# Kernel tuning notes

Hardware: AMD Instinct MI355X
Metric: run time of the kernel (lower is better)

Reference implementation:

```python
import jax, jax.numpy as jnp
import numpy as np

N_NODES = 100000


def sage_conv(x, edge_index, W_l, W_r, b):
    # PyG SAGEConv (aggr='mean', root_weight=True):
    # out_i = (mean_{j in N(i)} x_j) @ W_l + x_i @ W_r + b
    src, dst = edge_index[0], edge_index[1]
    msgs = x[src]                                             # [E, F] gather
    summed = jax.ops.segment_sum(msgs, dst, num_segments=N_NODES)
    deg = jax.ops.segment_sum(jnp.ones((edge_index.shape[1],), x.dtype), dst,
                              num_segments=N_NODES)
    mean = summed / jnp.maximum(deg, 1.0)[:, None]            # [N, F]
    return mean @ W_l + x @ W_r + b


def setup_inputs() -> dict:
    key = jax.random.key(0)
    ks = jax.random.split(key, 12)
    F, H = 128, 128
    E = 1600000
    s = lambda k, shp, fan: jax.random.normal(k, shp, jnp.float32) / np.sqrt(fan)
    return {
        "x": jax.random.normal(ks[0], (N_NODES, F), jnp.float32),
        "edge_index": jax.random.randint(ks[1], (2, E), 0, N_NODES, jnp.int64),
        "W1_l": s(ks[2], (F, H), F), "W1_r": s(ks[3], (F, H), F),
        "b1": jnp.zeros((H,), jnp.float32),
        "W2_l": s(ks[4], (H, H), H), "W2_r": s(ks[5], (H, H), H),
        "b2": jnp.zeros((H,), jnp.float32),
        "W3_l": s(ks[6], (H, 1), H), "W3_r": s(ks[7], (H, 1), H),
        "b3": jnp.zeros((1,), jnp.float32),
    }


def reference(x, edge_index, W1_l, W1_r, b1, W2_l, W2_r, b2, W3_l, W3_r, b3):
    h = jax.nn.relu(sage_conv(x, edge_index, W1_l, W1_r, b1))
    h = jax.nn.relu(sage_conv(h, edge_index, W2_l, W2_r, b2))
    h = sage_conv(h, edge_index, W3_l, W3_r, b3)   # [N, 1]
    return h.mean(axis=1)                          # [N]
```

## Files before the change

kernel.cpp:

```cpp
#include <hip/hip_runtime.h>


#define NN 100000
#define NB 391
#define SLAB 5120

typedef short bf16x8 __attribute__((ext_vector_type(8)));
typedef float f32x4 __attribute__((ext_vector_type(4)));

static __device__ __forceinline__ float uaf(unsigned u) { return __uint_as_float(u); }
static __device__ __forceinline__ unsigned short f2bf(float f) {
  unsigned u = __float_as_uint(f);
  u += 0x7fffu + ((u >> 16) & 1u);
  return (unsigned short)(u >> 16);
}

__global__ __launch_bounds__(256) void k_prep(
    const int* __restrict__ src, const int* __restrict__ dst, int E, int SB,
    int* __restrict__ cursor, unsigned* __restrict__ pairs,
    const float* __restrict__ x, unsigned short* __restrict__ Z1,
    unsigned short* __restrict__ Z2,
    const float* __restrict__ W1l, const float* __restrict__ W1r,
    const float* __restrict__ W2l, const float* __restrict__ W2r,
    unsigned short* __restrict__ wt1h, unsigned short* __restrict__ wt1l,
    unsigned short* __restrict__ wt2h, unsigned short* __restrict__ wt2l) {
  __shared__ int h[NB];
  __shared__ int rb[NB];
  const int b = blockIdx.x;
  const int tid = threadIdx.x;
  const int XB = NN * 16 / 256;

  if (b < SB) {
    for (int i = tid; i < NB; i += 256) h[i] = 0;
    __syncthreads();
    int s[8], d[8];
    const int base = b * 2048 + tid * 8;
    #pragma unroll
    for (int i = 0; i < 8; i++) {
      int g = base + i;
      bool ok = g < E;
      s[i] = ok ? src[g] : 0;
      d[i] = ok ? dst[g] : -1;
      if (ok) atomicAdd(&h[d[i] >> 8], 1);
    }
    __syncthreads();
    for (int i = tid; i < NB; i += 256) {
      rb[i] = h[i] ? atomicAdd(&cursor[i], h[i]) : 0;
      h[i] = 0;
    }
    __syncthreads();
    #pragma unroll
    for (int i = 0; i < 8; i++) {
      if (d[i] >= 0) {
        int bk = d[i] >> 8;
        int off = rb[bk] + atomicAdd(&h[bk], 1);
        if (off < SLAB)
          pairs[(size_t)bk * SLAB + off] =
              ((unsigned)(d[i] & 255) << 17) | (unsigned)s[i];
      }
    }
  } else if (b < SB + XB) {
    int t = (b - SB) * 256 + tid;
    int node = t >> 4, c = t & 15;
    const float4* xp = (const float4*)(x + (size_t)node * 128 + c * 8);
    float4 a = xp[0], bb = xp[1];
    float v[8] = {a.x, a.y, a.z, a.w, bb.x, bb.y, bb.z, bb.w};
    unsigned hh[8];
    #pragma unroll
    for (int i = 0; i < 8; i++) hh[i] = f2bf(v[i]);
    uint4 p;
    p.x = hh[0] | (hh[1] << 16); p.y = hh[2] | (hh[3] << 16);
    p.z = hh[4] | (hh[5] << 16); p.w = hh[6] | (hh[7] << 16);
    *(uint4*)(Z1 + (size_t)node * 256 + 128 + c * 8) = p;
  } else if (b < SB + XB + 64) {
    #pragma unroll
    for (int it = 0; it < 4; it++) {
      int t = (b - SB - XB) * 1024 + it * 256 + tid;
      int layer = t >> 15;
      int rem = t & 32767;
      int k = rem >> 7;
      int nn = rem & 127;
      const float* Wl = layer ? W2l : W1l;
      const float* Wr = layer ? W2r : W1r;
      float v = (k < 128) ? Wl[k * 128 + nn] : Wr[(k - 128) * 128 + nn];
      unsigned short hv = f2bf(v);
      unsigned short lv = f2bf(v - uaf(((unsigned)hv) << 16));
      const int frag = (nn >> 4) * 8 + (k >> 7) * 4 + ((k >> 5) & 3);
      const int lane = ((k >> 3) & 3) * 16 + (nn & 15);
      const int addr = frag * 512 + lane * 8 + (k & 7);
      (layer ? wt2h : wt1h)[addr] = hv;
      (layer ? wt2l : wt1l)[addr] = lv;
    }
  } else {
    unsigned* z1r = (unsigned*)(Z1 + (size_t)NN * 256);
    unsigned* z2r = (unsigned*)(Z2 + (size_t)NN * 256);
    if (tid < 128) z1r[tid] = 0;
    else z2r[tid - 128] = 0;
  }
}

__global__ __launch_bounds__(256) void k_build(const unsigned* __restrict__ pairs,
                                               const int* __restrict__ cursor,
                                               int* __restrict__ beg, int* __restrict__ deg,
                                               int* __restrict__ csr, int N) {
  __shared__ int cnt[256];
  __shared__ int sd[256];
  __shared__ int cur[256];
  const int b = blockIdx.x;
  const int tid = threadIdx.x;
  const size_t p0 = (size_t)b * SLAB;
  int count = cursor[b];
  if (count > SLAB) count = SLAB;
  cnt[tid] = 0;
  cur[tid] = 0;
  __syncthreads();
  for (int i = tid; i < count; i += 256) atomicAdd(&cnt[pairs[p0 + i] >> 17], 1);
  __syncthreads();
  int v = cnt[tid];
  sd[tid] = v;
  __syncthreads();
  #pragma unroll
  for (int off = 1; off < 256; off <<= 1) {
    int u = (tid >= off) ? sd[tid - off] : 0;
    __syncthreads();
    sd[tid] += u;
    __syncthreads();
  }
  const int node = b * 256 + tid;
  if (node < N) {
    beg[node] = (int)p0 + (sd[tid] - v);
    deg[node] = v;
  }
  __syncthreads();
  for (int i = tid; i < count; i += 256) {
    unsigned pv = pairs[p0 + i];
    int dl = pv >> 17;
    int pos = (sd[dl] - cnt[dl]) + atomicAdd(&cur[dl], 1);
    csr[p0 + pos] = pv & 0x1ffff;
  }
}

#define ACC8(v)                                   \
  acc[0] += uaf((v).x << 16);                     \
  acc[1] += uaf((v).x & 0xffff0000u);             \
  acc[2] += uaf((v).y << 16);                     \
  acc[3] += uaf((v).y & 0xffff0000u);             \
  acc[4] += uaf((v).z << 16);                     \
  acc[5] += uaf((v).z & 0xffff0000u);             \
  acc[6] += uaf((v).w << 16);                     \
  acc[7] += uaf((v).w & 0xffff0000u);

__global__ __launch_bounds__(256) void k_aggZ(unsigned short* __restrict__ Z,
                                              const int* __restrict__ begA,
                                              const int* __restrict__ degA,
                                              const int* __restrict__ csr, int n) {
  const int wid = (blockIdx.x * blockDim.x + threadIdx.x) >> 6;
  const int lane = threadIdx.x & 63;
  if (wid >= n) return;
  const int beg = begA[wid];
  const int d = degA[wid];
  const int g = lane >> 4, c = lane & 15;
  float acc[8] = {0.f, 0.f, 0.f, 0.f, 0.f, 0.f, 0.f, 0.f};

  for (int base = 0; base < d; base += 64) {
    int m = d - base;
    if (m > 64) m = 64;
    int idx = csr[beg + base + (lane < m ? lane : 0)];
    for (int k = 0; k < m; k += 32) {
      uint4 vA[4], vB[4];
      const bool hasB = (k + 16) < m;
      #pragma unroll
      for (int u = 0; u < 4; u++) {
        int kk = k + u * 4 + g;
        int j = __shfl(idx, kk & 63);
        j = (kk < m) ? j : NN;
        vA[u] = *(const uint4*)(Z + (size_t)j * 256 + 128 + c * 8);
      }
      if (hasB) {
        #pragma unroll
        for (int u = 0; u < 4; u++) {
          int kk = k + 16 + u * 4 + g;
          int j = __shfl(idx, kk & 63);
          j = (kk < m) ? j : NN;
          vB[u] = *(const uint4*)(Z + (size_t)j * 256 + 128 + c * 8);
        }
      }
      #pragma unroll
      for (int u = 0; u < 4; u++) { ACC8(vA[u]); }
      if (hasB) {
        #pragma unroll
        for (int u = 0; u < 4; u++) { ACC8(vB[u]); }
      }
    }
  }
  #pragma unroll
  for (int j = 0; j < 8; j++) {
    acc[j] += __shfl_xor(acc[j], 16);
    acc[j] += __shfl_xor(acc[j], 32);
  }
  const float inv = d > 0 ? 1.0f / (float)d : 0.f;
  if (g == 0) {
    unsigned h[8];
    #pragma unroll
    for (int j = 0; j < 8; j++) h[j] = f2bf(acc[j] * inv);
    uint4 p;
    p.x = h[0] | (h[1] << 16); p.y = h[2] | (h[3] << 16);
    p.z = h[4] | (h[5] << 16); p.w = h[6] | (h[7] << 16);
    *(uint4*)(Z + (size_t)wid * 256 + c * 8) = p;
  }
}

template <int MODE>
__global__ __launch_bounds__(256, 2) void k_sage2(
    const unsigned short* __restrict__ Z, const unsigned short* __restrict__ WTh,
    const unsigned short* __restrict__ WTl, const float* __restrict__ bias,
    unsigned short* __restrict__ outB,
    const float* __restrict__ w3l, const float* __restrict__ w3r,
    float* __restrict__ s2, float* __restrict__ r2, int n) {
  const int tid = threadIdx.x;
  const int lane = tid & 63;
  const int w = tid >> 6;
  const int ln = lane & 15;
  const int r16 = lane >> 4;
  const int m0 = blockIdx.x * 256 + w * 64;

  f32x4 acc[4][8];
  #pragma unroll
  for (int s = 0; s < 4; s++)
    #pragma unroll
    for (int cc = 0; cc < 8; cc++) {
      acc[s][cc][0] = 0.f; acc[s][cc][1] = 0.f;
      acc[s][cc][2] = 0.f; acc[s][cc][3] = 0.f;
    }
  float4 bv4[8];
  #pragma unroll
  for (int cc = 0; cc < 8; cc++) bv4[cc] = *(const float4*)(bias + cc * 16 + r16 * 4);

  #pragma unroll
  for (int kh = 0; kh < 2; kh++) {
    bf16x8 a[4][4];
    #pragma unroll
    for (int s = 0; s < 4; s++) {
      int row = m0 + s * 16 + ln;
      if (row > n - 1) row = n - 1;
      const unsigned short* zp = Z + (size_t)row * 256 + kh * 128 + r16 * 8;
      #pragma unroll
      for (int ks = 0; ks < 4; ks++) a[s][ks] = *(const bf16x8*)(zp + ks * 32);
    }
    #pragma unroll
    for (int ks = 0; ks < 4; ks++) {
      #pragma unroll
      for (int cg = 0; cg < 4; cg++) {
        bf16x8 bh[2], bl[2];
        #pragma unroll
        for (int j = 0; j < 2; j++) {
          const size_t o = (size_t)(((cg * 2 + j) * 8 + kh * 4 + ks) * 512 + lane * 8);
          bh[j] = *(const bf16x8*)(WTh + o);
          bl[j] = *(const bf16x8*)(WTl + o);
        }
        #pragma unroll
        for (int j = 0; j < 2; j++) {
          #pragma unroll
          for (int s = 0; s < 4; s++) {
            acc[s][cg * 2 + j] =
                __builtin_amdgcn_mfma_f32_16x16x32_bf16(bh[j], a[s][ks], acc[s][cg * 2 + j], 0, 0, 0);
            acc[s][cg * 2 + j] =
                __builtin_amdgcn_mfma_f32_16x16x32_bf16(bl[j], a[s][ks], acc[s][cg * 2 + j], 0, 0, 0);
          }
        }
      }
    }
  }

  if (MODE == 0) {
    #pragma unroll
    for (int s = 0; s < 4; s++) {
      const int node = m0 + s * 16 + ln;
      if (node < n) {
        unsigned short* op = outB + (size_t)node * 256 + 128 + r16 * 4;
        #pragma unroll
        for (int cc = 0; cc < 8; cc++) {
          ushort4 hq;
          hq.x = f2bf(fmaxf(acc[s][cc][0] + bv4[cc].x, 0.f));
          hq.y = f2bf(fmaxf(acc[s][cc][1] + bv4[cc].y, 0.f));
          hq.z = f2bf(fmaxf(acc[s][cc][2] + bv4[cc].z, 0.f));
          hq.w = f2bf(fmaxf(acc[s][cc][3] + bv4[cc].w, 0.f));
          *(ushort4*)(op + cc * 16) = hq;
        }
      }
    }
  } else {
    float4 wl4[8], wr4[8];
    #pragma unroll
    for (int cc = 0; cc < 8; cc++) {
      wl4[cc] = *(const float4*)(w3l + cc * 16 + r16 * 4);
      wr4[cc] = *(const float4*)(w3r + cc * 16 + r16 * 4);
    }
    #pragma unroll
    for (int s = 0; s < 4; s++) {
      float sl = 0.f, sr = 0.f;
      #pragma unroll
      for (int cc = 0; cc < 8; cc++) {
        float v0 = fmaxf(acc[s][cc][0] + bv4[cc].x, 0.f);
        float v1 = fmaxf(acc[s][cc][1] + bv4[cc].y, 0.f);
        float v2 = fmaxf(acc[s][cc][2] + bv4[cc].z, 0.f);
        float v3 = fmaxf(acc[s][cc][3] + bv4[cc].w, 0.f);
        sl += v0 * wl4[cc].x + v1 * wl4[cc].y + v2 * wl4[cc].z + v3 * wl4[cc].w;
        sr += v0 * wr4[cc].x + v1 * wr4[cc].y + v2 * wr4[cc].z + v3 * wr4[cc].w;
      }
      sl += __shfl_xor(sl, 16); sl += __shfl_xor(sl, 32);
      sr += __shfl_xor(sr, 16); sr += __shfl_xor(sr, 32);
      const int node = m0 + s * 16 + ln;
      if (r16 == 0 && node < n) {
        s2[node] = sl;
        r2[node] = sr;
      }
    }
  }
}

__global__ __launch_bounds__(256) void k_out3(const float* __restrict__ s2,
                                              const float* __restrict__ r2,
                                              const int* __restrict__ beg,
                                              const int* __restrict__ deg,
                                              const int* __restrict__ csr,
                                              const float* __restrict__ b3,
                                              float* __restrict__ out, int n) {
  int t = blockIdx.x * blockDim.x + threadIdx.x;
  int node = t >> 4;
  int ln = t & 15;
  if (node >= n) return;
  int bg = beg[node], d = deg[node];
  float s = 0.f;
  for (int i = ln; i < d; i += 16) s += s2[csr[bg + i]];
  s += __shfl_xor(s, 1); s += __shfl_xor(s, 2);
  s += __shfl_xor(s, 4); s += __shfl_xor(s, 8);
  if (ln == 0) out[node] = s / (d > 0 ? (float)d : 1.0f) + r2[node] + b3[0];
}

extern "C" void kernel_launch(void* const* d_in, const int* in_sizes, int n_in,
                              void* d_out, int out_size, void* d_ws, size_t ws_size,
                              hipStream_t stream) {
  const float* x   = (const float*)d_in[0];
  const int*   ei  = (const int*)d_in[1];
  const float* W1l = (const float*)d_in[2];
  const float* W1r = (const float*)d_in[3];
  const float* b1  = (const float*)d_in[4];
  const float* W2l = (const float*)d_in[5];
  const float* W2r = (const float*)d_in[6];
  const float* b2  = (const float*)d_in[7];
  const float* W3l = (const float*)d_in[8];
  const float* W3r = (const float*)d_in[9];
  const float* b3  = (const float*)d_in[10];
  float* out = (float*)d_out;

  const int N = NN;
  const int E = in_sizes[1] / 2;
  const int* src = ei;
  const int* dst = ei + E;

  char* ws = (char*)d_ws;
  size_t off = 0;
  auto alloc = [&](size_t bytes) -> char* {
    char* p = ws + off;
    off = (off + bytes + 255) & ~(size_t)255;
    return p;
  };
  int* cursor = (int*)alloc((NB + 1) * 4);
  unsigned* pairs = (unsigned*)alloc((size_t)NB * SLAB * 4);
  int* csr  = (int*)alloc(((size_t)NB * SLAB + 128) * 4);
  int* beg  = (int*)alloc((size_t)N * 4);
  int* deg  = (int*)alloc((size_t)N * 4);
  float* s2 = (float*)alloc((size_t)N * 4);
  float* r2 = (float*)alloc((size_t)N * 4);
  unsigned short* wt1h = (unsigned short*)alloc(128 * 256 * 2);
  unsigned short* wt1l = (unsigned short*)alloc(128 * 256 * 2);
  unsigned short* wt2h = (unsigned short*)alloc(128 * 256 * 2);
  unsigned short* wt2l = (unsigned short*)alloc(128 * 256 * 2);
  unsigned short* Z1 = (unsigned short*)alloc((size_t)(N + 1) * 256 * 2);
  unsigned short* Z2 = (unsigned short*)alloc((size_t)(N + 1) * 256 * 2);

  hipMemsetAsync(cursor, 0, (NB + 1) * 4, stream);

  const int SB = (E + 2047) / 2048;
  const int XB = N * 16 / 256;
  k_prep<<<SB + XB + 64 + 1, 256, 0, stream>>>(
      src, dst, E, SB, cursor, pairs, x, Z1, Z2,
      W1l, W1r, W2l, W2r, wt1h, wt1l, wt2h, wt2l);
  k_build<<<NB, 256, 0, stream>>>(pairs, cursor, beg, deg, csr, N);

  const int wb = (N * 64 + 255) / 256;
  const int sb = (N + 255) / 256;
  k_aggZ<<<wb, 256, 0, stream>>>(Z1, beg, deg, csr, N);
  k_sage2<0><<<sb, 256, 0, stream>>>(Z1, wt1h, wt1l, b1, Z2,
                                     nullptr, nullptr, nullptr, nullptr, N);
  k_aggZ<<<wb, 256, 0, stream>>>(Z2, beg, deg, csr, N);
  k_sage2<1><<<sb, 256, 0, stream>>>(Z2, wt2h, wt2l, b2, nullptr,
                                     W3l, W3r, s2, r2, N);
  k_out3<<<(N * 16 + 255) / 256, 256, 0, stream>>>(s2, r2, beg, deg, csr, b3, out, N);
}
```

Measured before the change: 248.6 us.

## Split aggregation feature halves across XCDs with persistent grid-stride waves

The aggregation kernel now splits the 128 features into two 64-wide halves. The half is chosen from the block's XCD index (blocks on XCDs 0-3 take the low half, 4-7 the high half), so each XCD's L2 caches only half of every gathered row. Each wave now handles 8 neighbours at once with 8 lanes per row. The launch uses a fixed 2048-block persistent grid that strides over nodes and prefetches the next node's degree and offset. This trades twice as many node visits and an extra shuffle-reduction step for better L2 hit rates on the random gathers, but it relies on the block-to-XCD round-robin assumption.

```diff
diff --git a/kernel.cpp b/kernel.cpp
--- a/kernel.cpp
+++ b/kernel.cpp
@@ -4,6 +4,8 @@
 #define NN 100000
 #define NB 391
 #define SLAB 5120
+#define AGG_BLOCKS 2048
+#define HALF_WAVES (AGG_BLOCKS / 8 * 4 * 4)
 
 typedef short bf16x8 __attribute__((ext_vector_type(8)));
 typedef float f32x4 __attribute__((ext_vector_type(4)));
@@ -154,35 +156,45 @@
                                               const int* __restrict__ begA,
                                               const int* __restrict__ degA,
                                               const int* __restrict__ csr, int n) {
-  const int wid = (blockIdx.x * blockDim.x + threadIdx.x) >> 6;
+  const int b = blockIdx.x;
+  const int xcd = b & 7;
+  const int F0 = (xcd >= 4) ? 64 : 0;
+  const int bh = (b >> 3) * 4 + (xcd & 3);
+  const int w = threadIdx.x >> 6;
+  const int hw = bh * 4 + w;
   const int lane = threadIdx.x & 63;
-  if (wid >= n) return;
-  const int beg = begA[wid];
-  const int d = degA[wid];
-  const int g = lane >> 4, c = lane & 15;
-  float acc[8] = {0.f, 0.f, 0.f, 0.f, 0.f, 0.f, 0.f, 0.f};
-
-  for (int base = 0; base < d; base += 64) {
-    int m = d - base;
-    if (m > 64) m = 64;
-    int idx = csr[beg + base + (lane < m ? lane : 0)];
-    for (int k = 0; k < m; k += 32) {
+  const int g = lane >> 3, c = lane & 7;
+
+  if (hw >= n) return;
+  int dP = degA[hw], bP = begA[hw];
+
+  for (int wid = hw; wid < n; wid += HALF_WAVES) {
+    const int d = dP;
+    const int beg = bP;
+    const int nw = wid + HALF_WAVES;
+    if (nw < n) { dP = degA[nw]; bP = begA[nw]; }
+    float acc[8] = {0.f, 0.f, 0.f, 0.f, 0.f, 0.f, 0.f, 0.f};
+
+    for (int base = 0; base < d; base += 64) {
+      int m = d - base;
+      if (m > 64) m = 64;
+      int idx = csr[beg + base + (lane < m ? lane : 0)];
       uint4 vA[4], vB[4];
-      const bool hasB = (k + 16) < m;
+      const bool hasB = m > 32;
       #pragma unroll
       for (int u = 0; u < 4; u++) {
-        int kk = k + u * 4 + g;
-        int j = __shfl(idx, kk & 63);
+        int kk = u * 8 + g;
+        int j = __shfl(idx, kk);
         j = (kk < m) ? j : NN;
-        vA[u] = *(const uint4*)(Z + (size_t)j * 256 + 128 + c * 8);
+        vA[u] = *(const uint4*)(Z + (size_t)j * 256 + 128 + F0 + c * 8);
       }
       if (hasB) {
         #pragma unroll
         for (int u = 0; u < 4; u++) {
-          int kk = k + 16 + u * 4 + g;
-          int j = __shfl(idx, kk & 63);
+          int kk = 32 + u * 8 + g;
+          int j = __shfl(idx, kk);
           j = (kk < m) ? j : NN;
-          vB[u] = *(const uint4*)(Z + (size_t)j * 256 + 128 + c * 8);
+          vB[u] = *(const uint4*)(Z + (size_t)j * 256 + 128 + F0 + c * 8);
         }
       }
       #pragma unroll
@@ -192,21 +204,22 @@
         for (int u = 0; u < 4; u++) { ACC8(vB[u]); }
       }
     }
-  }
-  #pragma unroll
-  for (int j = 0; j < 8; j++) {
-    acc[j] += __shfl_xor(acc[j], 16);
-    acc[j] += __shfl_xor(acc[j], 32);
-  }
-  const float inv = d > 0 ? 1.0f / (float)d : 0.f;
-  if (g == 0) {
-    unsigned h[8];
-    #pragma unroll
-    for (int j = 0; j < 8; j++) h[j] = f2bf(acc[j] * inv);
-    uint4 p;
-    p.x = h[0] | (h[1] << 16); p.y = h[2] | (h[3] << 16);
-    p.z = h[4] | (h[5] << 16); p.w = h[6] | (h[7] << 16);
-    *(uint4*)(Z + (size_t)wid * 256 + c * 8) = p;
+    #pragma unroll
+    for (int j = 0; j < 8; j++) {
+      acc[j] += __shfl_xor(acc[j], 8);
+      acc[j] += __shfl_xor(acc[j], 16);
+      acc[j] += __shfl_xor(acc[j], 32);
+    }
+    const float inv = d > 0 ? 1.0f / (float)d : 0.f;
+    if (g == 0) {
+      unsigned h[8];
+      #pragma unroll
+      for (int j = 0; j < 8; j++) h[j] = f2bf(acc[j] * inv);
+      uint4 p;
+      p.x = h[0] | (h[1] << 16); p.y = h[2] | (h[3] << 16);
+      p.z = h[4] | (h[5] << 16); p.w = h[6] | (h[7] << 16);
+      *(uint4*)(Z + (size_t)wid * 256 + F0 + c * 8) = p;
+    }
   }
 }
 
@@ -389,12 +402,11 @@
       W1l, W1r, W2l, W2r, wt1h, wt1l, wt2h, wt2l);
   k_build<<<NB, 256, 0, stream>>>(pairs, cursor, beg, deg, csr, N);
 
-  const int wb = (N * 64 + 255) / 256;
   const int sb = (N + 255) / 256;
-  k_aggZ<<<wb, 256, 0, stream>>>(Z1, beg, deg, csr, N);
+  k_aggZ<<<AGG_BLOCKS, 256, 0, stream>>>(Z1, beg, deg, csr, N);
   k_sage2<0><<<sb, 256, 0, stream>>>(Z1, wt1h, wt1l, b1, Z2,
                                      nullptr, nullptr, nullptr, nullptr, N);
-  k_aggZ<<<wb, 256, 0, stream>>>(Z2, beg, deg, csr, N);
+  k_aggZ<<<AGG_BLOCKS, 256, 0, stream>>>(Z2, beg, deg, csr, N);
   k_sage2<1><<<sb, 256, 0, stream>>>(Z2, wt2h, wt2l, b2, nullptr,
                                      W3l, W3r, s2, r2, N);
   k_out3<<<(N * 16 + 255) / 256, 256, 0, stream>>>(s2, r2, beg, deg, csr, b3, out, N);
```

Measured after the change: 316.1 us. +27.1%, slower.

## Split feature buffers into compact gather table and MFMA-fragment-ordered operands

Applied to the files above, without the earlier changes.

Replaces the interleaved [agg|root] 256-wide node rows with a compact 128-wide row-major table for neighbour gathers, plus separate buffers stored in MFMA fragment order for the aggregate and root operands. The gather kernel now reads half-width rows, which packs more nodes per cache line and may improve gather locality. The GEMM kernel loads A fragments with fully coalesced lane-contiguous reads instead of strided row loads. The trade-off is that each producer writes twice (row-major and fragment-ordered), there are extra tail memsets, and buffer aliasing is reused between layers.

```diff
diff --git a/kernel.cpp b/kernel.cpp
--- a/kernel.cpp
+++ b/kernel.cpp
@@ -4,6 +4,7 @@
 #define NN 100000
 #define NB 391
 #define SLAB 5120
+#define NGB 1563
 
 typedef short bf16x8 __attribute__((ext_vector_type(8)));
 typedef float f32x4 __attribute__((ext_vector_type(4)));
@@ -15,11 +16,16 @@
   return (unsigned short)(u >> 16);
 }
 
+static __device__ __forceinline__ size_t fo_addr16(int nd, int c) {
+  return (size_t)(nd >> 6) * 8192 + (size_t)(c >> 2) * 2048 +
+         (size_t)((nd >> 4) & 3) * 512 + (size_t)(((c & 3) << 4) + (nd & 15)) * 8;
+}
+
 __global__ __launch_bounds__(256) void k_prep(
     const int* __restrict__ src, const int* __restrict__ dst, int E, int SB,
     int* __restrict__ cursor, unsigned* __restrict__ pairs,
-    const float* __restrict__ x, unsigned short* __restrict__ Z1,
-    unsigned short* __restrict__ Z2,
+    const float* __restrict__ x, unsigned short* __restrict__ Zrm,
+    unsigned short* __restrict__ root1,
     const float* __restrict__ W1l, const float* __restrict__ W1r,
     const float* __restrict__ W2l, const float* __restrict__ W2r,
     unsigned short* __restrict__ wt1h, unsigned short* __restrict__ wt1l,
@@ -71,7 +77,8 @@
     uint4 p;
     p.x = hh[0] | (hh[1] << 16); p.y = hh[2] | (hh[3] << 16);
     p.z = hh[4] | (hh[5] << 16); p.w = hh[6] | (hh[7] << 16);
-    *(uint4*)(Z1 + (size_t)node * 256 + 128 + c * 8) = p;
+    *(uint4*)(Zrm + (size_t)node * 128 + c * 8) = p;
+    *(uint4*)(root1 + fo_addr16(node, c)) = p;
   } else if (b < SB + XB + 64) {
     #pragma unroll
     for (int it = 0; it < 4; it++) {
@@ -92,10 +99,8 @@
       (layer ? wt2l : wt1l)[addr] = lv;
     }
   } else {
-    unsigned* z1r = (unsigned*)(Z1 + (size_t)NN * 256);
-    unsigned* z2r = (unsigned*)(Z2 + (size_t)NN * 256);
-    if (tid < 128) z1r[tid] = 0;
-    else z2r[tid - 128] = 0;
+    unsigned* zr = (unsigned*)(Zrm + (size_t)NN * 128);
+    if (tid < 64) zr[tid] = 0;
   }
 }
 
@@ -150,7 +155,8 @@
   acc[6] += uaf((v).w << 16);                     \
   acc[7] += uaf((v).w & 0xffff0000u);
 
-__global__ __launch_bounds__(256) void k_aggZ(unsigned short* __restrict__ Z,
+__global__ __launch_bounds__(256) void k_aggZ(const unsigned short* __restrict__ Zrm,
+                                              unsigned short* __restrict__ aggfo,
                                               const int* __restrict__ begA,
                                               const int* __restrict__ degA,
                                               const int* __restrict__ csr, int n) {
@@ -174,7 +180,7 @@
         int kk = k + u * 4 + g;
         int j = __shfl(idx, kk & 63);
         j = (kk < m) ? j : NN;
-        vA[u] = *(const uint4*)(Z + (size_t)j * 256 + 128 + c * 8);
+        vA[u] = *(const uint4*)(Zrm + (size_t)j * 128 + c * 8);
       }
       if (hasB) {
         #pragma unroll
@@ -182,7 +188,7 @@
           int kk = k + 16 + u * 4 + g;
           int j = __shfl(idx, kk & 63);
           j = (kk < m) ? j : NN;
-          vB[u] = *(const uint4*)(Z + (size_t)j * 256 + 128 + c * 8);
+          vB[u] = *(const uint4*)(Zrm + (size_t)j * 128 + c * 8);
         }
       }
       #pragma unroll
@@ -206,15 +212,16 @@
     uint4 p;
     p.x = h[0] | (h[1] << 16); p.y = h[2] | (h[3] << 16);
     p.z = h[4] | (h[5] << 16); p.w = h[6] | (h[7] << 16);
-    *(uint4*)(Z + (size_t)wid * 256 + c * 8) = p;
+    *(uint4*)(aggfo + fo_addr16(wid, c)) = p;
   }
 }
 
 template <int MODE>
 __global__ __launch_bounds__(256, 2) void k_sage2(
-    const unsigned short* __restrict__ Z, const unsigned short* __restrict__ WTh,
-    const unsigned short* __restrict__ WTl, const float* __restrict__ bias,
-    unsigned short* __restrict__ outB,
+    const unsigned short* __restrict__ aggfo, const unsigned short* __restrict__ rootfo,
+    const unsigned short* __restrict__ WTh, const unsigned short* __restrict__ WTl,
+    const float* __restrict__ bias,
+    unsigned short* __restrict__ Zrm_out, unsigned short* __restrict__ rootfo_out,
     const float* __restrict__ w3l, const float* __restrict__ w3r,
     float* __restrict__ s2, float* __restrict__ r2, int n) {
   const int tid = threadIdx.x;
@@ -223,6 +230,7 @@
   const int ln = lane & 15;
   const int r16 = lane >> 4;
   const int m0 = blockIdx.x * 256 + w * 64;
+  const size_t fbase = (size_t)(m0 >> 6) * 8192;
 
   f32x4 acc[4][8];
   #pragma unroll
@@ -238,15 +246,13 @@
 
   #pragma unroll
   for (int kh = 0; kh < 2; kh++) {
+    const unsigned short* zf = kh ? rootfo : aggfo;
     bf16x8 a[4][4];
     #pragma unroll
-    for (int s = 0; s < 4; s++) {
-      int row = m0 + s * 16 + ln;
-      if (row > n - 1) row = n - 1;
-      const unsigned short* zp = Z + (size_t)row * 256 + kh * 128 + r16 * 8;
+    for (int ks = 0; ks < 4; ks++)
       #pragma unroll
-      for (int ks = 0; ks < 4; ks++) a[s][ks] = *(const bf16x8*)(zp + ks * 32);
-    }
+      for (int s = 0; s < 4; s++)
+        a[s][ks] = *(const bf16x8*)(zf + fbase + (size_t)ks * 2048 + s * 512 + lane * 8);
     #pragma unroll
     for (int ks = 0; ks < 4; ks++) {
       #pragma unroll
@@ -277,7 +283,7 @@
     for (int s = 0; s < 4; s++) {
       const int node = m0 + s * 16 + ln;
       if (node < n) {
-        unsigned short* op = outB + (size_t)node * 256 + 128 + r16 * 4;
+        unsigned short* op = Zrm_out + (size_t)node * 128 + r16 * 4;
         #pragma unroll
         for (int cc = 0; cc < 8; cc++) {
           ushort4 hq;
@@ -286,6 +292,10 @@
           hq.z = f2bf(fmaxf(acc[s][cc][2] + bv4[cc].z, 0.f));
           hq.w = f2bf(fmaxf(acc[s][cc][3] + bv4[cc].w, 0.f));
           *(ushort4*)(op + cc * 16) = hq;
+          const size_t fo = fbase + (size_t)(cc >> 1) * 2048 + (size_t)s * 512 +
+                            (size_t)((((cc & 1) * 2 + (r16 >> 1)) << 4) + ln) * 8 +
+                            (r16 & 1) * 4;
+          *(ushort4*)(rootfo_out + fo) = hq;
         }
       }
     }
@@ -377,25 +387,32 @@
   unsigned short* wt1l = (unsigned short*)alloc(128 * 256 * 2);
   unsigned short* wt2h = (unsigned short*)alloc(128 * 256 * 2);
   unsigned short* wt2l = (unsigned short*)alloc(128 * 256 * 2);
-  unsigned short* Z1 = (unsigned short*)alloc((size_t)(N + 1) * 256 * 2);
-  unsigned short* Z2 = (unsigned short*)alloc((size_t)(N + 1) * 256 * 2);
+  unsigned short* Zrm   = (unsigned short*)alloc((size_t)(N + 1) * 128 * 2);
+  unsigned short* root1 = (unsigned short*)alloc((size_t)NGB * 8192 * 2);
+  unsigned short* agg1  = (unsigned short*)alloc((size_t)NGB * 8192 * 2);
+  unsigned short* root2 = (unsigned short*)alloc((size_t)NGB * 8192 * 2);
+  unsigned short* agg2  = root1;
 
   hipMemsetAsync(cursor, 0, (NB + 1) * 4, stream);
+  const size_t tail = (size_t)(NGB - 1) * 8192 * 2;
+  hipMemsetAsync((char*)root1 + tail, 0, 8192 * 2, stream);
+  hipMemsetAsync((char*)agg1 + tail, 0, 8192 * 2, stream);
+  hipMemsetAsync((char*)root2 + tail, 0, 8192 * 2, stream);
 
   const int SB = (E + 2047) / 2048;
   const int XB = N * 16 / 256;
   k_prep<<<SB + XB + 64 + 1, 256, 0, stream>>>(
-      src, dst, E, SB, cursor, pairs, x, Z1, Z2,
+      src, dst, E, SB, cursor, pairs, x, Zrm, root1,
       W1l, W1r, W2l, W2r, wt1h, wt1l, wt2h, wt2l);
   k_build<<<NB, 256, 0, stream>>>(pairs, cursor, beg, deg, csr, N);
 
   const int wb = (N * 64 + 255) / 256;
   const int sb = (N + 255) / 256;
-  k_aggZ<<<wb, 256, 0, stream>>>(Z1, beg, deg, csr, N);
-  k_sage2<0><<<sb, 256, 0, stream>>>(Z1, wt1h, wt1l, b1, Z2,
+  k_aggZ<<<wb, 256, 0, stream>>>(Zrm, agg1, beg, deg, csr, N);
+  k_sage2<0><<<sb, 256, 0, stream>>>(agg1, root1, wt1h, wt1l, b1, Zrm, root2,
                                      nullptr, nullptr, nullptr, nullptr, N);
-  k_aggZ<<<wb, 256, 0, stream>>>(Z2, beg, deg, csr, N);
-  k_sage2<1><<<sb, 256, 0, stream>>>(Z2, wt2h, wt2l, b2, nullptr,
+  k_aggZ<<<wb, 256, 0, stream>>>(Zrm, agg2, beg, deg, csr, N);
+  k_sage2<1><<<sb, 256, 0, stream>>>(agg2, root2, wt2h, wt2l, b2, nullptr, nullptr,
                                      W3l, W3r, s2, r2, N);
   k_out3<<<(N * 16 + 255) / 256, 256, 0, stream>>>(s2, r2, beg, deg, csr, b3, out, N);
 }
```

Result: slower. 260.1 us (+4.6%).
